# Kernel optimization log

Measured on AMD Instinct MI355X. Metric: run time of the kernel, lower is better.

Reference implementation:

```python
import jax, jax.numpy as jnp
import numpy as np

N, E = 50000, 800000
IN, HID, OUT, EH = 128, 64, 128, 32  # node dims, edge-MLP hidden=32
N_ETYPES, N_NTYPES = 3, 2


def setup_inputs() -> dict:
    key = jax.random.key(0)
    ks = jax.random.split(key, 12)
    w = lambda k, shape, fan: jax.random.normal(k, shape, jnp.float32) / np.float32(np.sqrt(fan))
    nf = jax.random.normal(ks[0], (N, IN), jnp.float32)
    edge_index = jax.random.randint(ks[1], (2, E), 0, N, dtype=jnp.int32)
    edge_type = jax.random.randint(ks[2], (E,), 0, N_ETYPES, dtype=jnp.int32)
    node_type = jax.random.randint(ks[3], (N,), 0, N_NTYPES, dtype=jnp.int32)
    return {
        "nf": nf,
        "edge_index": edge_index,
        "edge_type": edge_type,
        "node_type": node_type,
        # layer 0: 128 -> 64
        "eW0": w(ks[4], (N_ETYPES, 2 * IN, EH), 2 * IN),
        "eb0": jax.random.normal(ks[5], (N_ETYPES, EH), jnp.float32) * 0.01,
        "nW0": w(ks[6], (N_NTYPES, N_ETYPES * EH, HID), N_ETYPES * EH),
        "nb0": jax.random.normal(ks[7], (N_NTYPES, HID), jnp.float32) * 0.01,
        # layer 1: 64 -> 128
        "eW1": w(ks[8], (N_ETYPES, 2 * HID, EH), 2 * HID),
        "eb1": jax.random.normal(ks[9], (N_ETYPES, EH), jnp.float32) * 0.01,
        "nW1": w(ks[10], (N_NTYPES, N_ETYPES * EH, OUT), N_ETYPES * EH),
        "nb1": jax.random.normal(ks[11], (N_NTYPES, OUT), jnp.float32) * 0.01,
    }


def _layer(nf, eW, eb, nW, nb, src, dst, edge_type, node_type):
    """One GraphNeuralNetLayer: per-edge-type message MLP + mean-scatter, then per-node-type update MLP."""
    n = nf.shape[0]
    # edge gather + concat: [E, 2*in]
    feat = jnp.concatenate([nf[src], nf[dst]], axis=-1)
    msgs = []
    for e in range(eW.shape[0]):  # fixed, small number of edge types
        m = jax.nn.relu(feat @ eW[e] + eb[e])            # [E, EH]
        mask = (edge_type == e).astype(nf.dtype)          # select this edge type
        s = jax.ops.segment_sum(m * mask[:, None], dst, num_segments=n)
        cnt = jax.ops.segment_sum(mask, dst, num_segments=n)
        # mean over mailbox; nodes with no type-e in-edges get zeros
        msgs.append(s / jnp.maximum(cnt, 1.0)[:, None])
    h = jnp.concatenate(msgs, axis=-1)                    # [N, 3*EH]
    out0 = jax.nn.relu(h @ nW[0] + nb[0])
    out1 = jax.nn.relu(h @ nW[1] + nb[1])
    return jnp.where((node_type == 0)[:, None], out0, out1)


def reference(nf, edge_index, edge_type, node_type, eW0, eb0, nW0, nb0, eW1, eb1, nW1, nb1):
    src, dst = edge_index[0], edge_index[1]
    h = _layer(nf, eW0, eb0, nW0, nb0, src, dst, edge_type, node_type)   # [N, 64]
    return _layer(h, eW1, eb1, nW1, nb1, src, dst, edge_type, node_type) # [N, 128]
```

## Files before the change

kernel.cpp:

```cpp
#include <hip/hip_runtime.h>


typedef __attribute__((ext_vector_type(8))) short bf16x8_t;
typedef __attribute__((ext_vector_type(4))) float f32x4_t;
typedef _Float16 f16;
typedef __attribute__((ext_vector_type(4))) _Float16 f16x4_t;
typedef __attribute__((ext_vector_type(8))) _Float16 f16x8_t;

__device__ __forceinline__ void cvt_split(float x, unsigned short& h, unsigned short& l) {
  unsigned u = __float_as_uint(x);
  unsigned rh = u + 0x7FFFu + ((u >> 16) & 1u);
  h = (unsigned short)(rh >> 16);
  float xh = __uint_as_float((unsigned)h << 16);
  float xl = x - xh;
  unsigned v = __float_as_uint(xl);
  unsigned rl = v + 0x7FFFu + ((v >> 16) & 1u);
  l = (unsigned short)(rl >> 16);
}


template <int IN, int OUT>
__device__ __forceinline__ void prep_dev(int id,
                                         const float* __restrict__ eW,
                                         float* __restrict__ wfh,
                                         float* __restrict__ wfl,
                                         const float* __restrict__ nW,
                                         float* __restrict__ wnh,
                                         float* __restrict__ wnl) {
  constexpr int KC = IN / 32;
  constexpr int CT = OUT / 16;
  if (id < 12 * KC * 64) {
    int lane = id & 63;
    int fk = id >> 6;
    int kc = fk % KC, ct = fk / KC;
    int n = ct * 16 + (lane & 15);
    int kb = kc * 32 + ((lane >> 4) & 3) * 8;
    int half = (n >= 96) ? 1 : 0;
    int jj = n - 96 * half;
    int e = jj >> 5, o = jj & 31;
    const float* wp = eW + ((size_t)((e * 2 + half) * IN) + kb) * 32 + o;
    bf16x8_t hv, lv;
#pragma unroll
    for (int j = 0; j < 8; ++j) {
      unsigned short h, l;
      cvt_split(wp[(size_t)j * 32], h, l);
      hv[j] = (short)h;
      lv[j] = (short)l;
    }
    *(bf16x8_t*)(wfh + (size_t)id * 4) = hv;
    *(bf16x8_t*)(wfl + (size_t)id * 4) = lv;
    return;
  }
  int id2 = id - 12 * KC * 64;
  if (id2 >= 2 * CT * 3 * 64) return;
  int lane = id2 & 63;
  int fk = id2 >> 6;
  int kc = fk % 3;
  int ct = (fk / 3) % CT;
  int t = fk / (3 * CT);
  const float* wp = nW + ((size_t)t * 96 + kc * 32 + ((lane >> 4) & 3) * 8) * OUT +
                    ct * 16 + (lane & 15);
  bf16x8_t hv, lv;
#pragma unroll
  for (int j = 0; j < 8; ++j) {
    unsigned short h, l;
    cvt_split(wp[(size_t)j * OUT], h, l);
    hv[j] = (short)h;
    lv[j] = (short)l;
  }
  *(bf16x8_t*)(wnh + (size_t)id2 * 4) = hv;
  *(bf16x8_t*)(wnl + (size_t)id2 * 4) = lv;
}

__global__ __launch_bounds__(256) void prep_all(const float* __restrict__ eW0,
                                                float* __restrict__ wf0h, float* __restrict__ wf0l,
                                                const float* __restrict__ nW1,
                                                float* __restrict__ wn1h, float* __restrict__ wn1l,
                                                const float* __restrict__ eW1,
                                                float* __restrict__ wf1h, float* __restrict__ wf1l,
                                                const float* __restrict__ nW0,
                                                float* __restrict__ wn0h, float* __restrict__ wn0l,
                                                int* __restrict__ deg8, int zn4,
                                                int* __restrict__ tcnt,
                                                int* __restrict__ gsum) {
  int bid = blockIdx.x;
  if (bid < 24) {
    int id = bid * 256 + threadIdx.x;
    int4* zb = (int4*)deg8;
    for (int z = id; z < zn4; z += 24 * 256) zb[z] = make_int4(0, 0, 0, 0);
    if (id < 2) tcnt[id] = 0;
    if (id == 2) gsum[0] = 0;
    prep_dev<128, 128>(id, eW0, wf0h, wf0l, nW1, wn1h, wn1l);
  } else {
    int id = (bid - 24) * 256 + threadIdx.x;
    prep_dev<64, 64>(id, eW1, wf1h, wf1l, nW0, wn0h, wn0l);
  }
}


template <int IN>
__device__ __forceinline__ void proj_dev(int bid,
                                         const float* __restrict__ X,
                                         const float* __restrict__ wfh,
                                         const float* __restrict__ wfl,
                                         f16* __restrict__ P, int n) {
  constexpr int KC = IN / 32;
  __shared__ short Ah[4 * KC * 64 * 8];
  __shared__ short Al[4 * KC * 64 * 8];
  const int tx = threadIdx.x;
  const int base = bid * 64;

  for (int q = tx; q < 4 * KC * 64; q += 256) {
    int lane = q & 63;
    int fk = q >> 6;
    int kc = fk % KC, nt = fk / KC;
    int node = base + nt * 16 + (lane & 15);
    int kb = kc * 32 + ((lane >> 4) & 3) * 8;
    float xs[8];
    if (node < n) {
      float4 a = *(const float4*)(X + (size_t)node * IN + kb);
      float4 b = *(const float4*)(X + (size_t)node * IN + kb + 4);
      xs[0] = a.x; xs[1] = a.y; xs[2] = a.z; xs[3] = a.w;
      xs[4] = b.x; xs[5] = b.y; xs[6] = b.z; xs[7] = b.w;
    } else {
#pragma unroll
      for (int j = 0; j < 8; ++j) xs[j] = 0.f;
    }
    bf16x8_t hv, lv;
#pragma unroll
    for (int j = 0; j < 8; ++j) {
      unsigned short h, l;
      cvt_split(xs[j], h, l);
      hv[j] = (short)h;
      lv[j] = (short)l;
    }
    *(bf16x8_t*)(Ah + (size_t)q * 8) = hv;
    *(bf16x8_t*)(Al + (size_t)q * 8) = lv;
  }
  __syncthreads();

  const int wave = tx >> 6;
  const int lane = tx & 63;

  f32x4_t acc[4][3];
#pragma unroll
  for (int nt = 0; nt < 4; ++nt)
#pragma unroll
    for (int c = 0; c < 3; ++c) acc[nt][c] = (f32x4_t){0.f, 0.f, 0.f, 0.f};

  for (int kc = 0; kc < KC; ++kc) {
    bf16x8_t Bh[3], Bl[3];
#pragma unroll
    for (int c = 0; c < 3; ++c) {
      int ct = wave * 3 + c;
      size_t idx = ((size_t)(ct * KC + kc) * 64 + lane) * 4;
      Bh[c] = *(const bf16x8_t*)(wfh + idx);
      Bl[c] = *(const bf16x8_t*)(wfl + idx);
    }
#pragma unroll
    for (int nt = 0; nt < 4; ++nt) {
      size_t idx = ((size_t)(nt * KC + kc) * 64 + lane) * 8;
      bf16x8_t ah = *(const bf16x8_t*)(Ah + idx);
      bf16x8_t al = *(const bf16x8_t*)(Al + idx);
#pragma unroll
      for (int c = 0; c < 3; ++c) {
        acc[nt][c] = __builtin_amdgcn_mfma_f32_16x16x32_bf16(ah, Bh[c], acc[nt][c], 0, 0, 0);
        acc[nt][c] = __builtin_amdgcn_mfma_f32_16x16x32_bf16(ah, Bl[c], acc[nt][c], 0, 0, 0);
        acc[nt][c] = __builtin_amdgcn_mfma_f32_16x16x32_bf16(al, Bh[c], acc[nt][c], 0, 0, 0);
      }
    }
  }

  const int row0 = ((lane >> 4) & 3) * 4;
  const int col = lane & 15;
#pragma unroll
  for (int nt = 0; nt < 4; ++nt) {
#pragma unroll
    for (int c = 0; c < 3; ++c) {
      int jcol = (wave * 3 + c) * 16 + col;
#pragma unroll
      for (int r = 0; r < 4; ++r) {
        int node = base + nt * 16 + row0 + r;
        if (node < n) P[(size_t)node * 192 + jcol] = (f16)acc[nt][c][r];
      }
    }
  }
}

template <int IN>
__global__ __launch_bounds__(256) void proj_mfma(const float* __restrict__ X,
                                                 const float* __restrict__ wfh,
                                                 const float* __restrict__ wfl,
                                                 f16* __restrict__ P, int n) {
  proj_dev<IN>(blockIdx.x, X, wfh, wfl, P, n);
}


__global__ __launch_bounds__(256) void fusedA(const float* __restrict__ X,
                                              const float* __restrict__ wfh,
                                              const float* __restrict__ wfl,
                                              f16* __restrict__ P, int n,
                                              int npb, int pbase,
                                              const int* __restrict__ dst,
                                              int* __restrict__ deg8,
                                              int* __restrict__ rank, int E, int egrid,
                                              const int* __restrict__ ntype,
                                              int* __restrict__ idxbuf,
                                              int* __restrict__ tcnt, int ncap) {
  int bid = blockIdx.x;
  int pb = bid / 9;
  if ((bid % 9) == 0 && pb < npb) {
    proj_dev<128>(pbase + pb, X, wfh, wfl, P, n);
    return;
  }
  int nproj_before = (bid % 9 == 0) ? pb : (pb + 1);
  if (nproj_before > npb) nproj_before = npb;
  int j = bid - nproj_before;
  if (j < egrid) {
    int i = j * 256 + threadIdx.x;
    if (i < E) {
      int d = dst[i];
      int r = (i >> 8) & 7;
      rank[i] = atomicAdd(&deg8[d * 8 + r], 1);
    }
    return;
  }
  j -= egrid;
  int i = j * 256 + threadIdx.x;
  int lane = threadIdx.x & 63;
  int t = (i < n) ? ntype[i] : -1;
  unsigned long long m0 = __ballot(t == 0);
  unsigned long long m1 = __ballot(t == 1);
  int b0 = 0, b1 = 0;
  if (lane == 0) {
    b0 = atomicAdd(&tcnt[0], (int)__popcll(m0));
    b1 = atomicAdd(&tcnt[1], (int)__popcll(m1));
  }
  b0 = __shfl(b0, 0);
  b1 = __shfl(b1, 0);
  unsigned long long below = (1ull << lane) - 1ull;
  if (t == 0) idxbuf[b0 + (int)__popcll(m0 & below)] = i;
  else if (t == 1) idxbuf[ncap + b1 + (int)__popcll(m1 & below)] = i;
}


__global__ __launch_bounds__(256) void scan_abs_kernel(int* __restrict__ deg8,
                                                       int* __restrict__ rowstart,
                                                       int* __restrict__ rowend,
                                                       int* __restrict__ gsum, int n) {
  __shared__ int tmp[256];
  __shared__ int bbs;
  int t = threadIdx.x;
  int base = blockIdx.x * 1024 + t * 4;
  int vdeg[4];
  int4 pa[4], pb[4];
#pragma unroll
  for (int q = 0; q < 4; ++q) {
    int v = base + q;
    int d = 0;
    int4 a = make_int4(0, 0, 0, 0), b = make_int4(0, 0, 0, 0);
    if (v < n) {
      a = *(int4*)(deg8 + (size_t)v * 8);
      b = *(int4*)(deg8 + (size_t)v * 8 + 4);
      int p1 = a.x, p2 = p1 + a.y, p3 = p2 + a.z, p4 = p3 + a.w;
      int p5 = p4 + b.x, p6 = p5 + b.y, p7 = p6 + b.z;
      d = p7 + b.w;
      a = make_int4(0, p1, p2, p3);
      b = make_int4(p4, p5, p6, p7);
    }
    pa[q] = a; pb[q] = b; vdeg[q] = d;
  }
  int s = vdeg[0] + vdeg[1] + vdeg[2] + vdeg[3];
  tmp[t] = s;
  __syncthreads();
  for (int off = 1; off < 256; off <<= 1) {
    int u = (t >= off) ? tmp[t - off] : 0;
    __syncthreads();
    tmp[t] += u;
    __syncthreads();
  }
  int excl = tmp[t] - s;
  if (t == 255) bbs = atomicAdd(gsum, tmp[255]);
  __syncthreads();
  int st = bbs + excl;
#pragma unroll
  for (int q = 0; q < 4; ++q) {
    int v = base + q;
    if (v < n) {
      rowstart[v] = st;
      rowend[v] = st + vdeg[q];
      int4 a = pa[q], b = pb[q];
      a.x += st; a.y += st; a.z += st; a.w += st;
      b.x += st; b.y += st; b.z += st; b.w += st;
      *(int4*)(deg8 + (size_t)v * 8) = a;
      *(int4*)(deg8 + (size_t)v * 8 + 4) = b;
    }
    st += vdeg[q];
  }
}


__global__ __launch_bounds__(256) void fusedB(const float* __restrict__ X,
                                              const float* __restrict__ wfh,
                                              const float* __restrict__ wfl,
                                              f16* __restrict__ P, int n,
                                              int npb, int pbase,
                                              const int* __restrict__ src,
                                              const int* __restrict__ dst,
                                              const int* __restrict__ etype,
                                              const int* __restrict__ rank,
                                              const int* __restrict__ deg8,
                                              int* __restrict__ edata, int E) {
  int bid = blockIdx.x;
  int pb = bid / 9;
  if ((bid % 9) == 0 && pb < npb) {
    proj_dev<128>(pbase + pb, X, wfh, wfl, P, n);
    return;
  }
  int nproj_before = (bid % 9 == 0) ? pb : (pb + 1);
  if (nproj_before > npb) nproj_before = npb;
  int j = bid - nproj_before;
  int i = j * 256 + threadIdx.x;
  if (i < E) {
    int d = dst[i];
    int r = (i >> 8) & 7;
    int et = etype[i];
    int pos = deg8[d * 8 + r] + rank[i];
    edata[pos] = src[i] * 384 + et * 65;
  }
}


#define ACC_EDGEH(pk, v)                                              \
  {                                                                   \
    int et_ = (pk) & 3;                                               \
    bool e0_ = (et_ == 0), e1_ = (et_ == 1), e2_ = (et_ == 2);        \
    _Pragma("unroll")                                                 \
    for (int j = 0; j < 4; ++j) {                                     \
      float pb_ = e0_ ? pdb0[j] : (e1_ ? pdb1[j] : pdb2[j]);          \
      float m_ = fmaxf((float)(v)[j] + pb_, 0.f);                     \
      a0[j] += e0_ ? m_ : 0.f;                                        \
      a1[j] += e1_ ? m_ : 0.f;                                        \
      a2[j] += e2_ ? m_ : 0.f;                                        \
    }                                                                 \
    c0 += e0_; c1 += e1_;                                             \
  }

__global__ __launch_bounds__(256) void aggregate_kernel(const f16* __restrict__ P,
                                                        const int* __restrict__ rowstart,
                                                        const int* __restrict__ rowend,
                                                        const int* __restrict__ edata,
                                                        const float* __restrict__ eb,
                                                        f16* __restrict__ h, int n) {
  int wid = (blockIdx.x * 256 + threadIdx.x) >> 6;
  if (wid >= n) return;
  int lane = threadIdx.x & 63;
  int co = (lane & 7) * 4;
  int cb = co * 2;
  int slot = lane >> 3;
  const f16* Pd = P + (size_t)wid * 192 + 96;
  float pdb0[4], pdb1[4], pdb2[4];
  {
    f16x4_t d0 = *(const f16x4_t*)(Pd + co);
    f16x4_t d1 = *(const f16x4_t*)(Pd + 32 + co);
    f16x4_t d2 = *(const f16x4_t*)(Pd + 64 + co);
    float4 e0 = *(const float4*)(eb + co);
    float4 e1 = *(const float4*)(eb + 32 + co);
    float4 e2 = *(const float4*)(eb + 64 + co);
    pdb0[0] = (float)d0[0] + e0.x; pdb0[1] = (float)d0[1] + e0.y;
    pdb0[2] = (float)d0[2] + e0.z; pdb0[3] = (float)d0[3] + e0.w;
    pdb1[0] = (float)d1[0] + e1.x; pdb1[1] = (float)d1[1] + e1.y;
    pdb1[2] = (float)d1[2] + e1.z; pdb1[3] = (float)d1[3] + e1.w;
    pdb2[0] = (float)d2[0] + e2.x; pdb2[1] = (float)d2[1] + e2.y;
    pdb2[2] = (float)d2[2] + e2.z; pdb2[3] = (float)d2[3] + e2.w;
  }
  int s = rowstart[wid];
  int e = rowend[wid];
  const char* Pb = (const char*)P;
  float a0[4], a1[4], a2[4];
#pragma unroll
  for (int j = 0; j < 4; ++j) { a0[j] = 0.f; a1[j] = 0.f; a2[j] = 0.f; }
  int c0 = 0, c1 = 0;
  for (int i = s + slot; i < e; i += 16) {
    int p0 = edata[i];
    int p1 = 3;
    int ii = i + 8;
    if (ii < e) p1 = edata[ii];
    f16x4_t v0 = *(const f16x4_t*)(Pb + (size_t)(p0 & ~3) + cb);
    f16x4_t v1 = *(const f16x4_t*)(Pb + (size_t)(p1 & ~3) + cb);
    ACC_EDGEH(p0, v0)
    ACC_EDGEH(p1, v1)
  }
#pragma unroll
  for (int off = 8; off < 64; off <<= 1) {
#pragma unroll
    for (int j = 0; j < 4; ++j) {
      a0[j] += __shfl_xor(a0[j], off);
      a1[j] += __shfl_xor(a1[j], off);
      a2[j] += __shfl_xor(a2[j], off);
    }
    c0 += __shfl_xor(c0, off);
    c1 += __shfl_xor(c1, off);
  }
  if (slot == 0) {
    int total = e - s;
    float d0 = fmaxf((float)c0, 1.f);
    float d1 = fmaxf((float)c1, 1.f);
    float d2 = fmaxf((float)(total - c0 - c1), 1.f);
    f16* hn = h + (size_t)wid * 96;
    f16x4_t o0, o1, o2;
#pragma unroll
    for (int j = 0; j < 4; ++j) {
      o0[j] = (f16)(a0[j] / d0);
      o1[j] = (f16)(a1[j] / d1);
      o2[j] = (f16)(a2[j] / d2);
    }
    *(f16x4_t*)(hn + co)      = o0;
    *(f16x4_t*)(hn + 32 + co) = o1;
    *(f16x4_t*)(hn + 64 + co) = o2;
  }
}


template <int OUT>
__global__ __launch_bounds__(256) void mlp2_mfma(const f16* __restrict__ H,
                                                 const float* __restrict__ wnh,
                                                 const float* __restrict__ wnl,
                                                 const float* __restrict__ nb,
                                                 const int* __restrict__ idxbuf,
                                                 const int* __restrict__ tcnt,
                                                 float* __restrict__ out, int ncap) {
  constexpr int CT = OUT / 16;
  constexpr int CW = CT / 4;
  __shared__ short Ah[12 * 64 * 8];
  __shared__ short Al[12 * 64 * 8];

  int c0 = tcnt[0];
  int nb0 = (c0 + 63) >> 6;
  int t, base, cnt;
  if ((int)blockIdx.x < nb0) {
    t = 0; base = blockIdx.x << 6; cnt = c0;
  } else {
    t = 1; base = ((int)blockIdx.x - nb0) << 6; cnt = tcnt[1];
    if (base >= cnt) return;
  }
  const int* il = idxbuf + (size_t)t * ncap;
  const float* bias = nb + t * OUT;

  const int tx = threadIdx.x;
  for (int q = tx; q < 12 * 64; q += 256) {
    int lane = q & 63;
    int fk = q >> 6;
    int kc = fk % 3, mt = fk / 3;
    int slot = base + mt * 16 + (lane & 15);
    int kb = kc * 32 + ((lane >> 4) & 3) * 8;
    float xs[8];
    if (slot < cnt) {
      int row = il[slot];
      f16x8_t a = *(const f16x8_t*)(H + (size_t)row * 96 + kb);
#pragma unroll
      for (int j = 0; j < 8; ++j) xs[j] = (float)a[j];
    } else {
#pragma unroll
      for (int j = 0; j < 8; ++j) xs[j] = 0.f;
    }
    bf16x8_t hv, lv;
#pragma unroll
    for (int j = 0; j < 8; ++j) {
      unsigned short h, l;
      cvt_split(xs[j], h, l);
      hv[j] = (short)h;
      lv[j] = (short)l;
    }
    *(bf16x8_t*)(Ah + (size_t)q * 8) = hv;
    *(bf16x8_t*)(Al + (size_t)q * 8) = lv;
  }
  __syncthreads();

  const int wave = tx >> 6;
  const int lane = tx & 63;

  f32x4_t acc[4][CW];
#pragma unroll
  for (int mt = 0; mt < 4; ++mt)
#pragma unroll
    for (int c = 0; c < CW; ++c) acc[mt][c] = (f32x4_t){0.f, 0.f, 0.f, 0.f};

  for (int kc = 0; kc < 3; ++kc) {
    bf16x8_t Bh[CW], Bl[CW];
#pragma unroll
    for (int c = 0; c < CW; ++c) {
      int ct = wave * CW + c;
      size_t idx = ((size_t)((t * CT + ct) * 3 + kc) * 64 + lane) * 4;
      Bh[c] = *(const bf16x8_t*)(wnh + idx);
      Bl[c] = *(const bf16x8_t*)(wnl + idx);
    }
#pragma unroll
    for (int mt = 0; mt < 4; ++mt) {
      size_t idx = ((size_t)((mt * 3 + kc) * 64) + lane) * 8;
      bf16x8_t ah = *(const bf16x8_t*)(Ah + idx);
      bf16x8_t al = *(const bf16x8_t*)(Al + idx);
#pragma unroll
      for (int c = 0; c < CW; ++c) {
        acc[mt][c] = __builtin_amdgcn_mfma_f32_16x16x32_bf16(ah, Bh[c], acc[mt][c], 0, 0, 0);
        acc[mt][c] = __builtin_amdgcn_mfma_f32_16x16x32_bf16(ah, Bl[c], acc[mt][c], 0, 0, 0);
        acc[mt][c] = __builtin_amdgcn_mfma_f32_16x16x32_bf16(al, Bh[c], acc[mt][c], 0, 0, 0);
      }
    }
  }

  const int row0 = ((lane >> 4) & 3) * 4;
  const int col = lane & 15;
#pragma unroll
  for (int mt = 0; mt < 4; ++mt) {
#pragma unroll
    for (int c = 0; c < CW; ++c) {
      int jcol = (wave * CW + c) * 16 + col;
      float bj = bias[jcol];
#pragma unroll
      for (int r = 0; r < 4; ++r) {
        int slot = base + mt * 16 + row0 + r;
        if (slot < cnt) {
          int row = il[slot];
          out[(size_t)row * OUT + jcol] = fmaxf(acc[mt][c][r] + bj, 0.f);
        }
      }
    }
  }
}


extern "C" void kernel_launch(void* const* d_in, const int* in_sizes, int n_in,
                              void* d_out, int out_size, void* d_ws, size_t ws_size,
                              hipStream_t stream) {
  const float* nf    = (const float*)d_in[0];
  const int*   eidx  = (const int*)d_in[1];
  const int*   etype = (const int*)d_in[2];
  const int*   ntype = (const int*)d_in[3];
  const float* eW0   = (const float*)d_in[4];
  const float* eb0   = (const float*)d_in[5];
  const float* nW0   = (const float*)d_in[6];
  const float* nb0   = (const float*)d_in[7];
  const float* eW1   = (const float*)d_in[8];
  const float* eb1   = (const float*)d_in[9];
  const float* nW1   = (const float*)d_in[10];
  const float* nb1   = (const float*)d_in[11];
  const int N = in_sizes[3];
  const int E = in_sizes[2];
  const int* srcv = eidx;
  const int* dstv = eidx + E;

  float* ws  = (float*)d_ws;
  f16*   P   = (f16*)ws;
  f16*   h96 = (f16*)(ws + (size_t)N * 192);
  float* h64 = ws + (size_t)N * 192 + (size_t)N * 96;
  int* rowstart = (int*)(h64 + (size_t)N * 64);
  int* rowend   = rowstart + N;
  int* tcnt     = rowend + N;
  int* gsum     = tcnt + 2;
  int* idxbuf   = gsum + 2;
  int* edata    = idxbuf + 2 * N;
  float* wf0h   = (float*)(edata + E);
  float* wf0l   = wf0h + 12288;
  float* wf1h   = wf0l + 12288;
  float* wf1l   = wf1h + 6144;
  float* wn0h   = wf1l + 6144;
  float* wn0l   = wn0h + 6144;
  float* wn1h   = wn0l + 6144;
  float* wn1l   = wn1h + 12288;
  int* rank     = (int*)(ws + (size_t)N * 192);
  int* deg8     = (int*)h64;

  const int nsb = (N + 1023) / 1024;
  const int egrid = (E + 255) / 256;
  const int pargrid = (N + 255) / 256;
  const int pgrid = (N + 63) / 64;
  const int npbA = (pgrid + 1) / 2;
  const int npbB = pgrid - npbA;

  prep_all<<<36, 256, 0, stream>>>(eW0, wf0h, wf0l, nW1, wn1h, wn1l,
                                   eW1, wf1h, wf1l, nW0, wn0h, wn0l,
                                   deg8, N * 2, tcnt, gsum);
  fusedA<<<npbA + egrid + pargrid, 256, 0, stream>>>(
      nf, wf0h, wf0l, P, N, npbA, 0,
      dstv, deg8, rank, E, egrid,
      ntype, idxbuf, tcnt, N);
  scan_abs_kernel<<<nsb, 256, 0, stream>>>(deg8, rowstart, rowend, gsum, N);
  fusedB<<<npbB + egrid, 256, 0, stream>>>(
      nf, wf0h, wf0l, P, N, npbB, npbA,
      srcv, dstv, etype, rank, deg8, edata, E);

  int agrid = (N + 3) / 4;
  int mgrid = (N + 63) / 64 + 2;

  aggregate_kernel<<<agrid, 256, 0, stream>>>(P, rowstart, rowend, edata, eb0, h96, N);
  mlp2_mfma<64><<<mgrid, 256, 0, stream>>>(h96, wn0h, wn0l, nb0, idxbuf, tcnt, h64, N);
  proj_mfma<64><<<pgrid, 256, 0, stream>>>(h64, wf1h, wf1l, P, N);
  aggregate_kernel<<<agrid, 256, 0, stream>>>(P, rowstart, rowend, edata, eb1, h96, N);
  mlp2_mfma<128><<<mgrid, 256, 0, stream>>>(h96, wn1h, wn1l, nb1, idxbuf, tcnt, (float*)d_out, N);
}
```

Baseline: 280.4 us.

## Merge weight prep into fusedA and move all layer-0 projection to fusedB

Removes the separate prep_all launch and folds the weight splitting into fusedA, with the zeroing of deg8 and the counters done by hipMemsetAsync instead. All of the layer-0 projection blocks now run in fusedB, interleaved one per five blocks, since the projection needs the prepared weights that fusedA now produces. This cuts one kernel launch and rebalances work across the pre-scan stages. In exchange it adds two memset operations, and fusedB becomes heavier while fusedA becomes lighter.

```diff
diff --git a/kernel.cpp b/kernel.cpp
--- a/kernel.cpp
+++ b/kernel.cpp
@@ -72,31 +72,6 @@
   *(bf16x8_t*)(wnl + (size_t)id2 * 4) = lv;
 }
 
-__global__ __launch_bounds__(256) void prep_all(const float* __restrict__ eW0,
-                                                float* __restrict__ wf0h, float* __restrict__ wf0l,
-                                                const float* __restrict__ nW1,
-                                                float* __restrict__ wn1h, float* __restrict__ wn1l,
-                                                const float* __restrict__ eW1,
-                                                float* __restrict__ wf1h, float* __restrict__ wf1l,
-                                                const float* __restrict__ nW0,
-                                                float* __restrict__ wn0h, float* __restrict__ wn0l,
-                                                int* __restrict__ deg8, int zn4,
-                                                int* __restrict__ tcnt,
-                                                int* __restrict__ gsum) {
-  int bid = blockIdx.x;
-  if (bid < 24) {
-    int id = bid * 256 + threadIdx.x;
-    int4* zb = (int4*)deg8;
-    for (int z = id; z < zn4; z += 24 * 256) zb[z] = make_int4(0, 0, 0, 0);
-    if (id < 2) tcnt[id] = 0;
-    if (id == 2) gsum[0] = 0;
-    prep_dev<128, 128>(id, eW0, wf0h, wf0l, nW1, wn1h, wn1l);
-  } else {
-    int id = (bid - 24) * 256 + threadIdx.x;
-    prep_dev<64, 64>(id, eW1, wf1h, wf1l, nW0, wn0h, wn0l);
-  }
-}
-
 
 template <int IN>
 __device__ __forceinline__ void proj_dev(int bid,
@@ -196,51 +171,56 @@
 }
 
 
-__global__ __launch_bounds__(256) void fusedA(const float* __restrict__ X,
-                                              const float* __restrict__ wfh,
-                                              const float* __restrict__ wfl,
-                                              f16* __restrict__ P, int n,
-                                              int npb, int pbase,
+__global__ __launch_bounds__(256) void fusedA(const float* __restrict__ eW0,
+                                              float* __restrict__ wf0h, float* __restrict__ wf0l,
+                                              const float* __restrict__ nW1,
+                                              float* __restrict__ wn1h, float* __restrict__ wn1l,
+                                              const float* __restrict__ eW1,
+                                              float* __restrict__ wf1h, float* __restrict__ wf1l,
+                                              const float* __restrict__ nW0,
+                                              float* __restrict__ wn0h, float* __restrict__ wn0l,
                                               const int* __restrict__ dst,
                                               int* __restrict__ deg8,
-                                              int* __restrict__ rank, int E, int egrid,
+                                              int* __restrict__ rank, int E,
                                               const int* __restrict__ ntype,
                                               int* __restrict__ idxbuf,
-                                              int* __restrict__ tcnt, int ncap) {
+                                              int* __restrict__ tcnt, int n, int ncap,
+                                              int pargrid) {
   int bid = blockIdx.x;
-  int pb = bid / 9;
-  if ((bid % 9) == 0 && pb < npb) {
-    proj_dev<128>(pbase + pb, X, wfh, wfl, P, n);
+  if (bid < 24) {
+    prep_dev<128, 128>(bid * 256 + threadIdx.x, eW0, wf0h, wf0l, nW1, wn1h, wn1l);
     return;
   }
-  int nproj_before = (bid % 9 == 0) ? pb : (pb + 1);
-  if (nproj_before > npb) nproj_before = npb;
-  int j = bid - nproj_before;
-  if (j < egrid) {
-    int i = j * 256 + threadIdx.x;
-    if (i < E) {
-      int d = dst[i];
-      int r = (i >> 8) & 7;
-      rank[i] = atomicAdd(&deg8[d * 8 + r], 1);
-    }
+  if (bid < 36) {
+    prep_dev<64, 64>((bid - 24) * 256 + threadIdx.x, eW1, wf1h, wf1l, nW0, wn0h, wn0l);
     return;
   }
-  j -= egrid;
-  int i = j * 256 + threadIdx.x;
-  int lane = threadIdx.x & 63;
-  int t = (i < n) ? ntype[i] : -1;
-  unsigned long long m0 = __ballot(t == 0);
-  unsigned long long m1 = __ballot(t == 1);
-  int b0 = 0, b1 = 0;
-  if (lane == 0) {
-    b0 = atomicAdd(&tcnt[0], (int)__popcll(m0));
-    b1 = atomicAdd(&tcnt[1], (int)__popcll(m1));
-  }
-  b0 = __shfl(b0, 0);
-  b1 = __shfl(b1, 0);
-  unsigned long long below = (1ull << lane) - 1ull;
-  if (t == 0) idxbuf[b0 + (int)__popcll(m0 & below)] = i;
-  else if (t == 1) idxbuf[ncap + b1 + (int)__popcll(m1 & below)] = i;
+  bid -= 36;
+  if (bid < pargrid) {
+    int i = bid * 256 + threadIdx.x;
+    int lane = threadIdx.x & 63;
+    int t = (i < n) ? ntype[i] : -1;
+    unsigned long long m0 = __ballot(t == 0);
+    unsigned long long m1 = __ballot(t == 1);
+    int b0 = 0, b1 = 0;
+    if (lane == 0) {
+      b0 = atomicAdd(&tcnt[0], (int)__popcll(m0));
+      b1 = atomicAdd(&tcnt[1], (int)__popcll(m1));
+    }
+    b0 = __shfl(b0, 0);
+    b1 = __shfl(b1, 0);
+    unsigned long long below = (1ull << lane) - 1ull;
+    if (t == 0) idxbuf[b0 + (int)__popcll(m0 & below)] = i;
+    else if (t == 1) idxbuf[ncap + b1 + (int)__popcll(m1 & below)] = i;
+    return;
+  }
+  bid -= pargrid;
+  int i = bid * 256 + threadIdx.x;
+  if (i < E) {
+    int d = dst[i];
+    int r = (i >> 8) & 7;
+    rank[i] = atomicAdd(&deg8[d * 8 + r], 1);
+  }
 }
 
 
@@ -303,8 +283,7 @@
 __global__ __launch_bounds__(256) void fusedB(const float* __restrict__ X,
                                               const float* __restrict__ wfh,
                                               const float* __restrict__ wfl,
-                                              f16* __restrict__ P, int n,
-                                              int npb, int pbase,
+                                              f16* __restrict__ P, int n, int npb,
                                               const int* __restrict__ src,
                                               const int* __restrict__ dst,
                                               const int* __restrict__ etype,
@@ -312,12 +291,12 @@
                                               const int* __restrict__ deg8,
                                               int* __restrict__ edata, int E) {
   int bid = blockIdx.x;
-  int pb = bid / 9;
-  if ((bid % 9) == 0 && pb < npb) {
-    proj_dev<128>(pbase + pb, X, wfh, wfl, P, n);
+  int pb = bid / 5;
+  if ((bid % 5) == 0 && pb < npb) {
+    proj_dev<128>(pb, X, wfh, wfl, P, n);
     return;
   }
-  int nproj_before = (bid % 9 == 0) ? pb : (pb + 1);
+  int nproj_before = (bid % 5 == 0) ? pb : (pb + 1);
   if (nproj_before > npb) nproj_before = npb;
   int j = bid - nproj_before;
   int i = j * 256 + threadIdx.x;
@@ -575,19 +554,17 @@
   const int egrid = (E + 255) / 256;
   const int pargrid = (N + 255) / 256;
   const int pgrid = (N + 63) / 64;
-  const int npbA = (pgrid + 1) / 2;
-  const int npbB = pgrid - npbA;
-
-  prep_all<<<36, 256, 0, stream>>>(eW0, wf0h, wf0l, nW1, wn1h, wn1l,
-                                   eW1, wf1h, wf1l, nW0, wn0h, wn0l,
-                                   deg8, N * 2, tcnt, gsum);
-  fusedA<<<npbA + egrid + pargrid, 256, 0, stream>>>(
-      nf, wf0h, wf0l, P, N, npbA, 0,
-      dstv, deg8, rank, E, egrid,
-      ntype, idxbuf, tcnt, N);
+
+  hipMemsetAsync(deg8, 0, (size_t)N * 8 * sizeof(int), stream);
+  hipMemsetAsync(tcnt, 0, 4 * sizeof(int), stream);
+  fusedA<<<36 + pargrid + egrid, 256, 0, stream>>>(
+      eW0, wf0h, wf0l, nW1, wn1h, wn1l,
+      eW1, wf1h, wf1l, nW0, wn0h, wn0l,
+      dstv, deg8, rank, E,
+      ntype, idxbuf, tcnt, N, N, pargrid);
   scan_abs_kernel<<<nsb, 256, 0, stream>>>(deg8, rowstart, rowend, gsum, N);
-  fusedB<<<npbB + egrid, 256, 0, stream>>>(
-      nf, wf0h, wf0l, P, N, npbB, npbA,
+  fusedB<<<pgrid + egrid, 256, 0, stream>>>(
+      nf, wf0h, wf0l, P, N, pgrid,
       srcv, dstv, etype, rank, deg8, edata, E);
 
   int agrid = (N + 3) / 4;
```

Result: no change. 278.3 us (-0.8%).
